# Performance work log

Hardware: AMD Instinct MI355X
Metric: run time of the kernel (lower is better)

The kernel has to match this reference:

```python
import jax, jax.numpy as jnp
import numpy as np

N, E, G = 100000, 800000, 64
F_IN, H = 92, 4
D1, D2, D3 = 32, 64, 128  # per-head out dims: hidden//2, hidden, 2*hidden
HID, LAT = 64, 128
FINAL = H * D3  # 512
NEG_SLOPE = 0.2


def _p(key, shape, scale=0.05):
    return jax.random.normal(key, shape, dtype=jnp.float32) * scale


def setup_inputs() -> dict:
    key = jax.random.key(0)
    ks = jax.random.split(key, 32)
    node_feat = jax.random.normal(ks[0], (N, F_IN), dtype=jnp.float32)
    src = jax.random.randint(ks[1], (E,), 0, N)
    dst = jax.random.randint(ks[2], (E,), 0, N)
    graph_id = jnp.sort(jax.random.randint(ks[3], (N,), 0, G))
    d = {"node_feat": node_feat, "src": src, "dst": dst, "graph_id": graph_id}
    # GAT layer params (DGL GATConv: fc no bias, attn_l/attn_r [H,D], bias [H*D])
    dims = [(F_IN, D1), (H * D1, D2), (H * D2, D3)]
    i = 4
    for li, (fi, do) in enumerate(dims, 1):
        d[f"W{li}"] = _p(ks[i], (fi, H * do)); i += 1
        d[f"al{li}"] = _p(ks[i], (H, do)); i += 1
        d[f"ar{li}"] = _p(ks[i], (H, do)); i += 1
        d[f"b{li}"] = jnp.zeros((H * do,), dtype=jnp.float32)
    # gate MLP: Linear(final, hid) -> ReLU -> Linear(hid, 1)
    d["Wg1"] = _p(ks[i], (FINAL, HID)); i += 1
    d["bg1"] = jnp.zeros((HID,), dtype=jnp.float32)
    d["Wg2"] = _p(ks[i], (HID, 1)); i += 1
    d["bg2"] = jnp.zeros((1,), dtype=jnp.float32)
    d["Wmu"] = _p(ks[i], (FINAL, LAT)); i += 1
    d["bmu"] = jnp.zeros((LAT,), dtype=jnp.float32)
    d["Wlv"] = _p(ks[i], (FINAL, LAT)); i += 1
    d["blv"] = jnp.zeros((LAT,), dtype=jnp.float32)
    return d


def gat_layer(h, W, al, ar, b, src, dst, heads, d_out):
    n = h.shape[0]
    Wh = (h @ W).reshape(n, heads, d_out)                      # [N,H,D]
    el = jnp.einsum('nhd,hd->nh', Wh, al)                      # a_l . Wh
    er = jnp.einsum('nhd,hd->nh', Wh, ar)
    e = jax.nn.leaky_relu(el[src] + er[dst], NEG_SLOPE)        # [E,H]
    m = jax.ops.segment_max(e, dst, num_segments=n)
    m = jnp.where(jnp.isfinite(m), m, 0.0)                     # zero-in-degree guard
    ex = jnp.exp(e - m[dst])
    s = jax.ops.segment_sum(ex, dst, num_segments=n)
    a = ex / jnp.maximum(s[dst], 1e-9)                         # edge softmax
    msg = a[:, :, None] * Wh[src]                              # [E,H,D] (peak intermediate)
    out = jax.ops.segment_sum(msg, dst, num_segments=n)        # scatter-aggregate
    out = out + b.reshape(1, heads, d_out)
    return out.reshape(n, heads * d_out)                       # flatten(1)


def attention_pool(h, graph_id, Wg1, bg1, Wg2, bg2, num_graphs):
    gate = jax.nn.relu(h @ Wg1 + bg1) @ Wg2 + bg2              # [N,1]
    m = jax.ops.segment_max(gate, graph_id, num_segments=num_graphs)
    ex = jnp.exp(gate - m[graph_id])
    s = jax.ops.segment_sum(ex, graph_id, num_segments=num_graphs)
    a = ex / jnp.maximum(s[graph_id], 1e-9)                    # softmax over nodes per graph
    return jax.ops.segment_sum(a * h, graph_id, num_segments=num_graphs)  # [G,final]


def reference(node_feat, src, dst, graph_id,
              W1, al1, ar1, b1, W2, al2, ar2, b2, W3, al3, ar3, b3,
              Wg1, bg1, Wg2, bg2, Wmu, bmu, Wlv, blv):
    h = jax.nn.elu(gat_layer(node_feat, W1, al1, ar1, b1, src, dst, H, D1))
    h = jax.nn.elu(gat_layer(h, W2, al2, ar2, b2, src, dst, H, D2))
    h = jax.nn.elu(gat_layer(h, W3, al3, ar3, b3, src, dst, H, D3))
    g = attention_pool(h, graph_id, Wg1, bg1, Wg2, bg2, G)
    mu = g @ Wmu + bmu
    logvar = g @ Wlv + blv
    return (mu, logvar)
```

## Files before the change

### kernel.cpp

```cpp
#include <hip/hip_runtime.h>
#include <math.h>

#define NNODES 100000
#define NEDGES 800000
#define NGRAPH 64
#define NHEAD  4
#define FINALD 512
#define HIDG   64
#define LATD   128
#define K1P    96
#define NB_SCAN 98

typedef unsigned int uint;
typedef unsigned short ushort;
typedef __attribute__((ext_vector_type(8))) short bf16x8;
typedef __attribute__((ext_vector_type(4))) float f32x4;

__device__ __forceinline__ float bflo(uint u) { return __uint_as_float(u << 16); }
__device__ __forceinline__ float bfhi(uint u) { return __uint_as_float(u & 0xffff0000u); }
__device__ __forceinline__ ushort f2bf(float f) {
    uint u = __float_as_uint(f);
    return (ushort)((u + 0x7fffu + ((u >> 16) & 1u)) >> 16);
}
__device__ __forceinline__ uint pack2(float a, float b) {
    return (uint)f2bf(a) | ((uint)f2bf(b) << 16);
}

__global__ void init_kernel(int* __restrict__ deg, const int* __restrict__ gid,
                            int* __restrict__ gstart) {
    int i = blockIdx.x * blockDim.x + threadIdx.x;
    if (i < NNODES) deg[i] = 0;
    if (i <= NGRAPH) {
        int lo = 0, hi = NNODES;
        while (lo < hi) {
            int mid = (lo + hi) >> 1;
            if (gid[mid] < i) lo = mid + 1; else hi = mid;
        }
        gstart[i] = lo;
    }
}
__global__ void count_kernel(const int* __restrict__ dst, int* __restrict__ deg) {
    int e = blockIdx.x * blockDim.x + threadIdx.x;
    if (e < NEDGES) atomicAdd(&deg[dst[e]], 1);
}
__global__ __launch_bounds__(1024) void scan_block_kernel(const int* __restrict__ deg,
                                                          int* __restrict__ off,
                                                          int* __restrict__ bsum) {
    __shared__ int buf[1024];
    int t = threadIdx.x;
    int i = blockIdx.x * 1024 + t;
    int x = (i < NNODES) ? deg[i] : 0;
    buf[t] = x;
    __syncthreads();
    for (int s = 1; s < 1024; s <<= 1) {
        int v = (t >= s) ? buf[t - s] : 0;
        __syncthreads();
        buf[t] += v;
        __syncthreads();
    }
    if (i < NNODES) off[i] = buf[t] - x;
    if (t == 1023) bsum[blockIdx.x] = buf[1023];
}
__global__ __launch_bounds__(128) void scan_bsum_kernel(int* __restrict__ bsum) {
    __shared__ int buf[128];
    int t = threadIdx.x;
    int x = (t < NB_SCAN) ? bsum[t] : 0;
    buf[t] = x;
    __syncthreads();
    for (int s = 1; s < 128; s <<= 1) {
        int v = (t >= s) ? buf[t - s] : 0;
        __syncthreads();
        buf[t] += v;
        __syncthreads();
    }
    if (t < NB_SCAN) bsum[t] = buf[t] - x;
    if (t == 0) bsum[NB_SCAN] = buf[NB_SCAN - 1];
}
__global__ __launch_bounds__(1024) void scan_add_kernel(int* __restrict__ off,
                                                        const int* __restrict__ bsum,
                                                        int* __restrict__ cursor) {
    int i = blockIdx.x * 1024 + threadIdx.x;
    if (i < NNODES) {
        int v = off[i] + bsum[blockIdx.x];
        off[i] = v;
        cursor[i] = v;
    }
    if (i == 0) off[NNODES] = bsum[NB_SCAN];
}
__global__ void scatter_kernel(const int* __restrict__ src, const int* __restrict__ dst,
                               int* __restrict__ cursor, int* __restrict__ src_csr) {
    int e = blockIdx.x * blockDim.x + threadIdx.x;
    if (e >= NEDGES) return;
    int p = atomicAdd(&cursor[dst[e]], 1);
    src_csr[p] = src[e];
}

#define C1 (128 * K1P)
#define C2 (256 * 128)
#define C3 (512 * 256)
#define CG (64 * 512)
#define CX (NNODES * K1P)
#define CTOT (C1 + C2 + C3 + CG + CX + NNODES)
__global__ void conv_all_kernel(const float* __restrict__ W1, const float* __restrict__ W2,
                                const float* __restrict__ W3, const float* __restrict__ Wg1,
                                const float* __restrict__ nf,
                                ushort* __restrict__ Bt1, ushort* __restrict__ Bt2,
                                ushort* __restrict__ Bt3, ushort* __restrict__ Btg,
                                ushort* __restrict__ x0, float* __restrict__ gate) {
    int i = blockIdx.x * blockDim.x + threadIdx.x;
    if (i < C1) {
        int n = i / K1P, k = i - n * K1P;
        Bt1[i] = (k < 92) ? f2bf(W1[(size_t)k * 128 + n]) : (ushort)0;
        return;
    }
    i -= C1;
    if (i < C2) {
        int n = i >> 7, k = i & 127;
        Bt2[i] = f2bf(W2[(size_t)k * 256 + n]);
        return;
    }
    i -= C2;
    if (i < C3) {
        int n = i >> 8, k = i & 255;
        Bt3[i] = f2bf(W3[(size_t)k * 512 + n]);
        return;
    }
    i -= C3;
    if (i < CG) {
        int n = i >> 9, k = i & 511;
        Btg[i] = f2bf(Wg1[(size_t)k * 64 + n]);
        return;
    }
    i -= CG;
    if (i < CX) {
        int n = i / K1P, k = i - n * K1P;
        x0[i] = (k < 92) ? f2bf(nf[(size_t)n * 92 + k]) : (ushort)0;
        return;
    }
    i -= CX;
    if (i < NNODES) gate[i] = 0.f;
}

template <int BN, int MODE>
__global__ __launch_bounds__(256) void mfma_gemm(const ushort* __restrict__ A,
                                                 const ushort* __restrict__ Bt,
                                                 const float* __restrict__ bias,
                                                 ushort* __restrict__ C,
                                                 const float* __restrict__ Wg2,
                                                 float* __restrict__ gate,
                                                 int M, int K, int N) {
    constexpr int WNS = BN / 2;
    constexpr int NT = WNS / 16;
    __shared__ ushort Alds[128][40];
    __shared__ ushort Blds[BN][40];
    int tid = threadIdx.x;
    int wave = tid >> 6, lane = tid & 63;
    int wm = wave & 1, wn = wave >> 1;
    int quad = lane >> 4, l16 = lane & 15;
    int rowBase = blockIdx.y * 128;
    int colBase = blockIdx.x * BN;

    f32x4 acc[4][NT];
#pragma unroll
    for (int i = 0; i < 4; i++)
#pragma unroll
        for (int j = 0; j < NT; j++) acc[i][j] = (f32x4){0.f, 0.f, 0.f, 0.f};

    for (int k0 = 0; k0 < K; k0 += 32) {
        {
            int r = tid >> 1;
            int c0 = (tid & 1) * 8;
            int row = rowBase + r;
            uint4 v0 = make_uint4(0u, 0u, 0u, 0u);
            uint4 v1 = make_uint4(0u, 0u, 0u, 0u);
            if (row < M) {
                const ushort* ap = &A[(size_t)row * K + k0];
                v0 = *(const uint4*)&ap[c0];
                v1 = *(const uint4*)&ap[c0 + 16];
            }
            *(uint4*)&Alds[r][c0] = v0;
            *(uint4*)&Alds[r][c0 + 16] = v1;
        }
        if constexpr (BN == 128) {
            int r = tid >> 1;
            int c0 = (tid & 1) * 8;
            const ushort* bp = &Bt[(size_t)(colBase + r) * K + k0];
            *(uint4*)&Blds[r][c0] = *(const uint4*)&bp[c0];
            *(uint4*)&Blds[r][c0 + 16] = *(const uint4*)&bp[c0 + 16];
        } else {
            int r = tid >> 2, ch = tid & 3;
            uint4 v = *(const uint4*)&Bt[(size_t)(colBase + r) * K + k0 + ch * 8];
            *(uint4*)&Blds[r][ch * 8] = v;
        }
        __syncthreads();
        bf16x8 af[4], bf[NT];
#pragma unroll
        for (int i = 0; i < 4; i++)
            af[i] = *(const bf16x8*)&Alds[wm * 64 + i * 16 + l16][quad * 8];
#pragma unroll
        for (int j = 0; j < NT; j++)
            bf[j] = *(const bf16x8*)&Blds[wn * WNS + j * 16 + l16][quad * 8];
#pragma unroll
        for (int i = 0; i < 4; i++)
#pragma unroll
            for (int j = 0; j < NT; j++)
                acc[i][j] = __builtin_amdgcn_mfma_f32_16x16x32_bf16(af[i], bf[j], acc[i][j], 0, 0, 0);
        __syncthreads();
    }

    if constexpr (MODE == 0) {
#pragma unroll
        for (int i = 0; i < 4; i++) {
#pragma unroll
            for (int j = 0; j < NT; j++) {
                int col = colBase + wn * WNS + j * 16 + l16;
#pragma unroll
                for (int r = 0; r < 4; r++) {
                    int row = rowBase + wm * 64 + i * 16 + quad * 4 + r;
                    if (row < M) C[(size_t)row * N + col] = f2bf(acc[i][j][r]);
                }
            }
        }
    } else {
        float bb[NT], wg[NT];
#pragma unroll
        for (int j = 0; j < NT; j++) {
            int col = colBase + wn * WNS + j * 16 + l16;
            bb[j] = bias[col];
            wg[j] = Wg2[col];
        }
#pragma unroll
        for (int i = 0; i < 4; i++) {
            float pd[4] = {0.f, 0.f, 0.f, 0.f};
#pragma unroll
            for (int j = 0; j < NT; j++) {
#pragma unroll
                for (int r = 0; r < 4; r++) {
                    float x = fmaxf(acc[i][j][r] + bb[j], 0.f);
                    pd[r] = fmaf(x, wg[j], pd[r]);
                }
            }
#pragma unroll
            for (int m = 1; m < 16; m <<= 1)
#pragma unroll
                for (int r = 0; r < 4; r++)
                    pd[r] += __shfl_xor(pd[r], m, 64);
            if (l16 == 0) {
#pragma unroll
                for (int r = 0; r < 4; r++) {
                    int row = rowBase + wm * 64 + i * 16 + quad * 4 + r;
                    if (row < M) atomicAdd(&gate[row], pd[r]);
                }
            }
        }
    }
}

template <int HD>
__global__ __launch_bounds__(256) void eler_node(const ushort* __restrict__ Wh,
                                                 const float* __restrict__ al,
                                                 const float* __restrict__ ar,
                                                 float* __restrict__ el,
                                                 float* __restrict__ er) {
    constexpr int D = HD / NHEAD;
    constexpr int LPN = HD / 8;
    constexpr int S = D / 8;
    int n = blockIdx.x * 4 + (threadIdx.x >> 6);
    int lane = threadIdx.x & 63;
    float sl = 0.f, sr = 0.f;
    if (lane < LPN) {
        int d0 = lane * 8;
        uint4 v = *(const uint4*)&Wh[(size_t)n * HD + d0];
        float w0 = bflo(v.x), w1 = bfhi(v.x), w2 = bflo(v.y), w3 = bfhi(v.y);
        float w4 = bflo(v.z), w5 = bfhi(v.z), w6 = bflo(v.w), w7 = bfhi(v.w);
        float4 a0 = *(const float4*)&al[d0];
        float4 a1 = *(const float4*)&al[d0 + 4];
        float4 b0 = *(const float4*)&ar[d0];
        float4 b1 = *(const float4*)&ar[d0 + 4];
        sl = w0 * a0.x; sl = fmaf(w1, a0.y, sl); sl = fmaf(w2, a0.z, sl); sl = fmaf(w3, a0.w, sl);
        sl = fmaf(w4, a1.x, sl); sl = fmaf(w5, a1.y, sl); sl = fmaf(w6, a1.z, sl); sl = fmaf(w7, a1.w, sl);
        sr = w0 * b0.x; sr = fmaf(w1, b0.y, sr); sr = fmaf(w2, b0.z, sr); sr = fmaf(w3, b0.w, sr);
        sr = fmaf(w4, b1.x, sr); sr = fmaf(w5, b1.y, sr); sr = fmaf(w6, b1.z, sr); sr = fmaf(w7, b1.w, sr);
    }
#pragma unroll
    for (int o = S / 2; o > 0; o >>= 1) {
        sl += __shfl_down(sl, o, 64);
        sr += __shfl_down(sr, o, 64);
    }
    if (lane < LPN && (lane % S) == 0) {
        int h = lane / S;
        el[n * 4 + h] = sl;
        er[n * 4 + h] = sr;
    }
}

__global__ void attn_node(const int* __restrict__ src_csr, const int* __restrict__ off,
                          const float4* __restrict__ el4, const float4* __restrict__ er4,
                          float4* __restrict__ aw4, float4* __restrict__ nsum4) {
    int n = blockIdx.x * blockDim.x + threadIdx.x;
    if (n >= NNODES) return;
    int i0 = off[n], i1 = off[n + 1];
    float4 ern = er4[n];
    float m0 = -1e30f, m1 = -1e30f, m2 = -1e30f, m3 = -1e30f;
    for (int i = i0; i < i1; i += 8) {
        int cnt = i1 - i; if (cnt > 8) cnt = 8;
        int s8[8];
#pragma unroll
        for (int j = 0; j < 8; j++)
            if (j < cnt) s8[j] = src_csr[i + j];
        float4 e8[8];
#pragma unroll
        for (int j = 0; j < 8; j++)
            if (j < cnt) e8[j] = el4[s8[j]];
#pragma unroll
        for (int j = 0; j < 8; j++) {
            if (j < cnt) {
                float4 x = e8[j];
                x.x += ern.x; x.y += ern.y; x.z += ern.z; x.w += ern.w;
                x.x = (x.x >= 0.f) ? x.x : 0.2f * x.x;
                x.y = (x.y >= 0.f) ? x.y : 0.2f * x.y;
                x.z = (x.z >= 0.f) ? x.z : 0.2f * x.z;
                x.w = (x.w >= 0.f) ? x.w : 0.2f * x.w;
                aw4[i + j] = x;
                m0 = fmaxf(m0, x.x); m1 = fmaxf(m1, x.y);
                m2 = fmaxf(m2, x.z); m3 = fmaxf(m3, x.w);
            }
        }
    }
    float4 s = make_float4(0.f, 0.f, 0.f, 0.f);
    for (int i = i0; i < i1; i++) {
        float4 x = aw4[i];
        x.x = expf(x.x - m0); x.y = expf(x.y - m1);
        x.z = expf(x.z - m2); x.w = expf(x.w - m3);
        s.x += x.x; s.y += x.y; s.z += x.z; s.w += x.w;
        aw4[i] = x;
    }
    nsum4[n] = s;
}

__global__ __launch_bounds__(256) void gat_aggregate(const int* __restrict__ src_csr,
                                                     const int* __restrict__ off,
                                                     const ushort* __restrict__ Wh,
                                                     const float* __restrict__ aw,
                                                     const float* __restrict__ nsum,
                                                     const float* __restrict__ bias,
                                                     ushort* __restrict__ out,
                                                     int HD, int logHD8, int logD, int total8) {
    int idx = blockIdx.x * blockDim.x + threadIdx.x;
    if (idx >= total8) return;
    int n = idx >> logHD8;
    int d = (idx & ((1 << logHD8) - 1)) << 3;
    int h = d >> logD;
    int i0 = off[n], i1 = off[n + 1];
    float acc[8] = {0.f, 0.f, 0.f, 0.f, 0.f, 0.f, 0.f, 0.f};
    for (int i = i0; i < i1; i += 8) {
        int cnt = i1 - i; if (cnt > 8) cnt = 8;
        int s8[8]; float w8[8];
#pragma unroll
        for (int j = 0; j < 8; j++) {
            if (j < cnt) {
                s8[j] = src_csr[i + j];
                w8[j] = aw[(i + j) * 4 + h];
            }
        }
#pragma unroll
        for (int j = 0; j < 8; j++) {
            if (j < cnt) {
                uint4 v = *(const uint4*)&Wh[(size_t)s8[j] * HD + d];
                float w = w8[j];
                acc[0] = fmaf(w, bflo(v.x), acc[0]);
                acc[1] = fmaf(w, bfhi(v.x), acc[1]);
                acc[2] = fmaf(w, bflo(v.y), acc[2]);
                acc[3] = fmaf(w, bfhi(v.y), acc[3]);
                acc[4] = fmaf(w, bflo(v.z), acc[4]);
                acc[5] = fmaf(w, bfhi(v.z), acc[5]);
                acc[6] = fmaf(w, bflo(v.w), acc[6]);
                acc[7] = fmaf(w, bfhi(v.w), acc[7]);
            }
        }
    }
    float inv = 1.f / fmaxf(nsum[n * 4 + h], 1e-9f);
    float r[8];
#pragma unroll
    for (int j = 0; j < 8; j++) {
        float x = acc[j] * inv + bias[d + j];
        r[j] = (x > 0.f) ? x : (expf(x) - 1.f);
    }
    uint4 o;
    o.x = pack2(r[0], r[1]);
    o.y = pack2(r[2], r[3]);
    o.z = pack2(r[4], r[5]);
    o.w = pack2(r[6], r[7]);
    *(uint4*)&out[(size_t)n * HD + d] = o;
}

__global__ __launch_bounds__(256) void graph_softmax_kernel(const float* __restrict__ gate,
                                                            const int* __restrict__ gstart,
                                                            float* __restrict__ exn,
                                                            float* __restrict__ gsum) {
    int g = blockIdx.x, t = threadIdx.x;
    int n0 = gstart[g], n1 = gstart[g + 1];
    __shared__ float red[256];
    float m = -1e30f;
    for (int n = n0 + t; n < n1; n += 256) m = fmaxf(m, gate[n]);
    red[t] = m; __syncthreads();
    for (int s = 128; s > 0; s >>= 1) {
        if (t < s) red[t] = fmaxf(red[t], red[t + s]);
        __syncthreads();
    }
    m = red[0]; __syncthreads();
    float sum = 0.f;
    for (int n = n0 + t; n < n1; n += 256) {
        float v = expf(gate[n] - m);
        exn[n] = v;
        sum += v;
    }
    red[t] = sum; __syncthreads();
    for (int s = 128; s > 0; s >>= 1) {
        if (t < s) red[t] += red[t + s];
        __syncthreads();
    }
    if (t == 0) gsum[g] = red[0];
}

__global__ __launch_bounds__(128) void pool_partial(const ushort* __restrict__ h,
                                                    const float* __restrict__ exn,
                                                    const int* __restrict__ gstart,
                                                    float* __restrict__ partial) {
    int g = blockIdx.x, q = blockIdx.y;
    int n0 = gstart[g], n1 = gstart[g + 1];
    int len = n1 - n0;
    int chunk = (len + 3) >> 2;
    int s = n0 + q * chunk;
    int e = s + chunk; if (e > n1) e = n1;
    int d4 = threadIdx.x;
    const uint2* h2 = (const uint2*)h;
    float a0 = 0.f, a1 = 0.f, a2 = 0.f, a3 = 0.f;
    for (int n = s; n < e; n++) {
        float w = exn[n];
        uint2 v = h2[(size_t)n * 128 + d4];
        a0 = fmaf(w, bflo(v.x), a0);
        a1 = fmaf(w, bfhi(v.x), a1);
        a2 = fmaf(w, bflo(v.y), a2);
        a3 = fmaf(w, bfhi(v.y), a3);
    }
    *(float4*)&partial[((size_t)(g * 4 + q)) * FINALD + d4 * 4] = make_float4(a0, a1, a2, a3);
}

__global__ __launch_bounds__(128) void final_kernel(const float* __restrict__ partial,
                                                    const float* __restrict__ gsum,
                                                    const float* __restrict__ Wmu,
                                                    const float* __restrict__ bmu,
                                                    const float* __restrict__ Wlv,
                                                    const float* __restrict__ blv,
                                                    float* __restrict__ out) {
    int g = blockIdx.x, j = threadIdx.x;
    const float* p = partial + (size_t)g * 4 * FINALD;
    float am = 0.f, av = 0.f;
    for (int k = 0; k < FINALD; k++) {
        float pv = p[k] + p[FINALD + k] + p[2 * FINALD + k] + p[3 * FINALD + k];
        am = fmaf(pv, Wmu[k * LATD + j], am);
        av = fmaf(pv, Wlv[k * LATD + j], av);
    }
    float inv = 1.f / fmaxf(gsum[g], 1e-9f);
    out[g * LATD + j] = am * inv + bmu[j];
    out[NGRAPH * LATD + g * LATD + j] = av * inv + blv[j];
}

extern "C" void kernel_launch(void* const* d_in, const int* in_sizes, int n_in,
                              void* d_out, int out_size, void* d_ws, size_t ws_size,
                              hipStream_t stream) {
    (void)in_sizes; (void)n_in; (void)out_size; (void)ws_size;
    const float* node_feat = (const float*)d_in[0];
    const int* src = (const int*)d_in[1];
    const int* dst = (const int*)d_in[2];
    const int* gid = (const int*)d_in[3];
    const float* W[3]    = {(const float*)d_in[4],  (const float*)d_in[8],  (const float*)d_in[12]};
    const float* al[3]   = {(const float*)d_in[5],  (const float*)d_in[9],  (const float*)d_in[13]};
    const float* ar[3]   = {(const float*)d_in[6],  (const float*)d_in[10], (const float*)d_in[14]};
    const float* bias[3] = {(const float*)d_in[7],  (const float*)d_in[11], (const float*)d_in[15]};
    const float* Wg1 = (const float*)d_in[16];
    const float* bg1 = (const float*)d_in[17];
    const float* Wg2 = (const float*)d_in[18];
    const float* Wmu = (const float*)d_in[20];
    const float* bmu = (const float*)d_in[21];
    const float* Wlv = (const float*)d_in[22];
    const float* blv = (const float*)d_in[23];

    char* ws = (char*)d_ws;
    size_t woff = 0;
    auto carve = [&](size_t bytes) {
        void* p = ws + woff;
        woff = (woff + bytes + 255) & ~(size_t)255;
        return p;
    };
    ushort* hA      = (ushort*)carve((size_t)NNODES * 512 * 2);
    ushort* hB      = (ushort*)carve((size_t)NNODES * 512 * 2);
    float*  el      = (float*) carve((size_t)NNODES * 4 * 4);
    float*  er      = (float*) carve((size_t)NNODES * 4 * 4);
    float*  aw      = (float*) carve((size_t)NEDGES * 4 * 4);
    float*  nsum    = (float*) carve((size_t)NNODES * 4 * 4);
    int*    deg     = (int*)   carve((size_t)NNODES * 4);
    int*    off     = (int*)   carve((size_t)(NNODES + 1) * 4);
    int*    cursor  = (int*)   carve((size_t)NNODES * 4);
    int*    src_csr = (int*)   carve((size_t)NEDGES * 4);
    int*    bsum    = (int*)   carve((size_t)(NB_SCAN + 1) * 4);
    float*  gate    = (float*) carve((size_t)NNODES * 4);
    float*  exn     = (float*) carve((size_t)NNODES * 4);
    int*    gstart  = (int*)   carve((size_t)(NGRAPH + 1) * 4);
    float*  partial = (float*) carve((size_t)NGRAPH * 4 * FINALD * 4);
    float*  gsum    = (float*) carve((size_t)NGRAPH * 4);
    ushort* Bt1     = (ushort*)carve((size_t)128 * K1P * 2);
    ushort* Bt2     = (ushort*)carve((size_t)256 * 128 * 2);
    ushort* Bt3     = (ushort*)carve((size_t)512 * 256 * 2);
    ushort* Btg     = (ushort*)carve((size_t)64 * 512 * 2);
    ushort* x0      = hA;

    init_kernel<<<(NNODES + 255) / 256, 256, 0, stream>>>(deg, gid, gstart);
    count_kernel<<<(NEDGES + 255) / 256, 256, 0, stream>>>(dst, deg);
    scan_block_kernel<<<NB_SCAN, 1024, 0, stream>>>(deg, off, bsum);
    scan_bsum_kernel<<<1, 128, 0, stream>>>(bsum);
    scan_add_kernel<<<NB_SCAN, 1024, 0, stream>>>(off, bsum, cursor);
    scatter_kernel<<<(NEDGES + 255) / 256, 256, 0, stream>>>(src, dst, cursor, src_csr);
    conv_all_kernel<<<(CTOT + 255) / 256, 256, 0, stream>>>(
        W[0], W[1], W[2], Wg1, node_feat, Bt1, Bt2, Bt3, Btg, x0, gate);

    const int HDs[3]    = {128, 256, 512};
    const int logHD8[3] = {4, 5, 6};
    const int logD[3]   = {5, 6, 7};
    const int MB = (NNODES + 127) / 128;

    for (int l = 0; l < 3; l++) {
        int HD = HDs[l];
        if (l == 0)
            mfma_gemm<128, 0><<<dim3(1, MB), 256, 0, stream>>>(
                x0, Bt1, nullptr, hB, nullptr, nullptr, NNODES, K1P, 128);
        else if (l == 1)
            mfma_gemm<128, 0><<<dim3(2, MB), 256, 0, stream>>>(
                hA, Bt2, nullptr, hB, nullptr, nullptr, NNODES, 128, 256);
        else
            mfma_gemm<128, 0><<<dim3(4, MB), 256, 0, stream>>>(
                hA, Bt3, nullptr, hB, nullptr, nullptr, NNODES, 256, 512);
        if (l == 0)      eler_node<128><<<NNODES / 4, 256, 0, stream>>>(hB, al[l], ar[l], el, er);
        else if (l == 1) eler_node<256><<<NNODES / 4, 256, 0, stream>>>(hB, al[l], ar[l], el, er);
        else             eler_node<512><<<NNODES / 4, 256, 0, stream>>>(hB, al[l], ar[l], el, er);
        attn_node<<<(NNODES + 255) / 256, 256, 0, stream>>>(
            src_csr, off, (const float4*)el, (const float4*)er, (float4*)aw, (float4*)nsum);
        int total8 = NNODES * (HD / 8);
        gat_aggregate<<<(total8 + 255) / 256, 256, 0, stream>>>(
            src_csr, off, hB, aw, nsum, bias[l], hA, HD, logHD8[l], logD[l], total8);
    }

    mfma_gemm<64, 1><<<dim3(1, MB), 256, 0, stream>>>(
        hA, Btg, bg1, nullptr, Wg2, gate, NNODES, FINALD, HIDG);
    graph_softmax_kernel<<<NGRAPH, 256, 0, stream>>>(gate, gstart, exn, gsum);
    pool_partial<<<dim3(NGRAPH, 4), 128, 0, stream>>>(hA, exn, gstart, partial);
    final_kernel<<<NGRAPH, 128, 0, stream>>>(partial, gsum, Wmu, bmu, Wlv, blv, (float*)d_out);
}
```

Measured before the change: 889.0 us.

## Fuse edge softmax into aggregation with wave-per-node online softmax; widen pool split

Replaces the separate attn_node and gat_aggregate kernels with one attn_aggregate kernel that assigns a 64-lane wavefront to each destination node. The wave computes per-head max and sum with an online softmax and shuffle reductions, then recomputes edge weights on the fly while gathering neighbor features. This removes the per-edge attention buffer and its write/read round trip. Separately, the graph pooling is split into 16 partial chunks per graph instead of 4 to raise parallelism, with final_kernel reducing them through shared memory. The cost is recomputing exp and el gathers per lane, and lower per-thread work for small head dims.

```diff
diff --git a/kernel.cpp b/kernel.cpp
--- a/kernel.cpp
+++ b/kernel.cpp
@@ -10,6 +10,7 @@
 #define LATD   128
 #define K1P    96
 #define NB_SCAN 98
+#define PQ     16
 
 typedef unsigned int uint;
 typedef unsigned short ushort;
@@ -24,6 +25,9 @@
 }
 __device__ __forceinline__ uint pack2(float a, float b) {
     return (uint)f2bf(a) | ((uint)f2bf(b) << 16);
+}
+__device__ __forceinline__ float selh(float4 v, int h) {
+    return (h & 2) ? ((h & 1) ? v.w : v.z) : ((h & 1) ? v.y : v.x);
 }
 
 __global__ void init_kernel(int* __restrict__ deg, const int* __restrict__ gid,
@@ -294,104 +298,119 @@
     }
 }
 
-__global__ void attn_node(const int* __restrict__ src_csr, const int* __restrict__ off,
-                          const float4* __restrict__ el4, const float4* __restrict__ er4,
-                          float4* __restrict__ aw4, float4* __restrict__ nsum4) {
-    int n = blockIdx.x * blockDim.x + threadIdx.x;
-    if (n >= NNODES) return;
+template <int HD>
+__global__ __launch_bounds__(256) void attn_aggregate(const int* __restrict__ src_csr,
+                                                      const int* __restrict__ off,
+                                                      const ushort* __restrict__ Wh,
+                                                      const float4* __restrict__ el4,
+                                                      const float4* __restrict__ er4,
+                                                      const float* __restrict__ bias,
+                                                      ushort* __restrict__ out) {
+    constexpr int DPL = HD / 64;
+    int n = blockIdx.x * 4 + (threadIdx.x >> 6);
+    int lane = threadIdx.x & 63;
     int i0 = off[n], i1 = off[n + 1];
     float4 ern = er4[n];
-    float m0 = -1e30f, m1 = -1e30f, m2 = -1e30f, m3 = -1e30f;
-    for (int i = i0; i < i1; i += 8) {
-        int cnt = i1 - i; if (cnt > 8) cnt = 8;
-        int s8[8];
-#pragma unroll
-        for (int j = 0; j < 8; j++)
-            if (j < cnt) s8[j] = src_csr[i + j];
-        float4 e8[8];
-#pragma unroll
-        for (int j = 0; j < 8; j++)
-            if (j < cnt) e8[j] = el4[s8[j]];
-#pragma unroll
-        for (int j = 0; j < 8; j++) {
-            if (j < cnt) {
-                float4 x = e8[j];
-                x.x += ern.x; x.y += ern.y; x.z += ern.z; x.w += ern.w;
-                x.x = (x.x >= 0.f) ? x.x : 0.2f * x.x;
-                x.y = (x.y >= 0.f) ? x.y : 0.2f * x.y;
-                x.z = (x.z >= 0.f) ? x.z : 0.2f * x.z;
-                x.w = (x.w >= 0.f) ? x.w : 0.2f * x.w;
-                aw4[i + j] = x;
-                m0 = fmaxf(m0, x.x); m1 = fmaxf(m1, x.y);
-                m2 = fmaxf(m2, x.z); m3 = fmaxf(m3, x.w);
-            }
-        }
-    }
-    float4 s = make_float4(0.f, 0.f, 0.f, 0.f);
-    for (int i = i0; i < i1; i++) {
-        float4 x = aw4[i];
-        x.x = expf(x.x - m0); x.y = expf(x.y - m1);
-        x.z = expf(x.z - m2); x.w = expf(x.w - m3);
-        s.x += x.x; s.y += x.y; s.z += x.z; s.w += x.w;
-        aw4[i] = x;
-    }
-    nsum4[n] = s;
-}
-
-__global__ __launch_bounds__(256) void gat_aggregate(const int* __restrict__ src_csr,
-                                                     const int* __restrict__ off,
-                                                     const ushort* __restrict__ Wh,
-                                                     const float* __restrict__ aw,
-                                                     const float* __restrict__ nsum,
-                                                     const float* __restrict__ bias,
-                                                     ushort* __restrict__ out,
-                                                     int HD, int logHD8, int logD, int total8) {
-    int idx = blockIdx.x * blockDim.x + threadIdx.x;
-    if (idx >= total8) return;
-    int n = idx >> logHD8;
-    int d = (idx & ((1 << logHD8) - 1)) << 3;
-    int h = d >> logD;
-    int i0 = off[n], i1 = off[n + 1];
-    float acc[8] = {0.f, 0.f, 0.f, 0.f, 0.f, 0.f, 0.f, 0.f};
+
+    float m[4] = {-1e30f, -1e30f, -1e30f, -1e30f};
+    float s[4] = {0.f, 0.f, 0.f, 0.f};
+    for (int i = i0 + lane; i < i1; i += 64) {
+        float4 x = el4[src_csr[i]];
+        float xs[4] = {x.x + ern.x, x.y + ern.y, x.z + ern.z, x.w + ern.w};
+#pragma unroll
+        for (int c = 0; c < 4; c++) {
+            float v = (xs[c] >= 0.f) ? xs[c] : 0.2f * xs[c];
+            float M = fmaxf(m[c], v);
+            s[c] = s[c] * expf(m[c] - M) + expf(v - M);
+            m[c] = M;
+        }
+    }
+    float gm[4] = {m[0], m[1], m[2], m[3]};
+#pragma unroll
+    for (int o = 1; o < 64; o <<= 1)
+#pragma unroll
+        for (int c = 0; c < 4; c++)
+            gm[c] = fmaxf(gm[c], __shfl_xor(gm[c], o, 64));
+#pragma unroll
+    for (int c = 0; c < 4; c++) s[c] *= expf(m[c] - gm[c]);
+#pragma unroll
+    for (int o = 1; o < 64; o <<= 1)
+#pragma unroll
+        for (int c = 0; c < 4; c++)
+            s[c] += __shfl_xor(s[c], o, 64);
+
+    int h = (lane * DPL) / (HD / 4);
+    float mh  = (h & 2) ? ((h & 1) ? gm[3] : gm[2]) : ((h & 1) ? gm[1] : gm[0]);
+    float sh  = (h & 2) ? ((h & 1) ? s[3] : s[2]) : ((h & 1) ? s[1] : s[0]);
+    float erh = selh(ern, h);
+    float inv = 1.f / fmaxf(sh, 1e-9f);
+
+    int d = lane * DPL;
+    float acc[DPL];
+#pragma unroll
+    for (int j = 0; j < DPL; j++) acc[j] = 0.f;
     for (int i = i0; i < i1; i += 8) {
         int cnt = i1 - i; if (cnt > 8) cnt = 8;
         int s8[8]; float w8[8];
 #pragma unroll
+        for (int j = 0; j < 8; j++)
+            if (j < cnt) s8[j] = src_csr[i + j];
+#pragma unroll
         for (int j = 0; j < 8; j++) {
             if (j < cnt) {
-                s8[j] = src_csr[i + j];
-                w8[j] = aw[(i + j) * 4 + h];
+                float xs = selh(el4[s8[j]], h) + erh;
+                xs = (xs >= 0.f) ? xs : 0.2f * xs;
+                w8[j] = expf(xs - mh) * inv;
             }
         }
 #pragma unroll
         for (int j = 0; j < 8; j++) {
             if (j < cnt) {
-                uint4 v = *(const uint4*)&Wh[(size_t)s8[j] * HD + d];
+                const ushort* p = &Wh[(size_t)s8[j] * HD + d];
                 float w = w8[j];
-                acc[0] = fmaf(w, bflo(v.x), acc[0]);
-                acc[1] = fmaf(w, bfhi(v.x), acc[1]);
-                acc[2] = fmaf(w, bflo(v.y), acc[2]);
-                acc[3] = fmaf(w, bfhi(v.y), acc[3]);
-                acc[4] = fmaf(w, bflo(v.z), acc[4]);
-                acc[5] = fmaf(w, bfhi(v.z), acc[5]);
-                acc[6] = fmaf(w, bflo(v.w), acc[6]);
-                acc[7] = fmaf(w, bfhi(v.w), acc[7]);
+                if constexpr (DPL == 8) {
+                    uint4 v = *(const uint4*)p;
+                    acc[0] = fmaf(w, bflo(v.x), acc[0]);
+                    acc[1] = fmaf(w, bfhi(v.x), acc[1]);
+                    acc[2] = fmaf(w, bflo(v.y), acc[2]);
+                    acc[3] = fmaf(w, bfhi(v.y), acc[3]);
+                    acc[4] = fmaf(w, bflo(v.z), acc[4]);
+                    acc[5] = fmaf(w, bfhi(v.z), acc[5]);
+                    acc[6] = fmaf(w, bflo(v.w), acc[6]);
+                    acc[7] = fmaf(w, bfhi(v.w), acc[7]);
+                } else if constexpr (DPL == 4) {
+                    uint2 v = *(const uint2*)p;
+                    acc[0] = fmaf(w, bflo(v.x), acc[0]);
+                    acc[1] = fmaf(w, bfhi(v.x), acc[1]);
+                    acc[2] = fmaf(w, bflo(v.y), acc[2]);
+                    acc[3] = fmaf(w, bfhi(v.y), acc[3]);
+                } else {
+                    uint v = *(const uint*)p;
+                    acc[0] = fmaf(w, bflo(v), acc[0]);
+                    acc[1] = fmaf(w, bfhi(v), acc[1]);
+                }
             }
         }
     }
-    float inv = 1.f / fmaxf(nsum[n * 4 + h], 1e-9f);
-    float r[8];
-#pragma unroll
-    for (int j = 0; j < 8; j++) {
-        float x = acc[j] * inv + bias[d + j];
+    float r[DPL];
+#pragma unroll
+    for (int j = 0; j < DPL; j++) {
+        float x = acc[j] + bias[d + j];
         r[j] = (x > 0.f) ? x : (expf(x) - 1.f);
     }
-    uint4 o;
-    o.x = pack2(r[0], r[1]);
-    o.y = pack2(r[2], r[3]);
-    o.z = pack2(r[4], r[5]);
-    o.w = pack2(r[6], r[7]);
-    *(uint4*)&out[(size_t)n * HD + d] = o;
+    ushort* po = &out[(size_t)n * HD + d];
+    if constexpr (DPL == 8) {
+        uint4 o;
+        o.x = pack2(r[0], r[1]); o.y = pack2(r[2], r[3]);
+        o.z = pack2(r[4], r[5]); o.w = pack2(r[6], r[7]);
+        *(uint4*)po = o;
+    } else if constexpr (DPL == 4) {
+        uint2 o;
+        o.x = pack2(r[0], r[1]); o.y = pack2(r[2], r[3]);
+        *(uint2*)po = o;
+    } else {
+        *(uint*)po = pack2(r[0], r[1]);
+    }
 }
 
 __global__ __launch_bounds__(256) void graph_softmax_kernel(const float* __restrict__ gate,
@@ -430,7 +449,7 @@
     int g = blockIdx.x, q = blockIdx.y;
     int n0 = gstart[g], n1 = gstart[g + 1];
     int len = n1 - n0;
-    int chunk = (len + 3) >> 2;
+    int chunk = (len + PQ - 1) / PQ;
     int s = n0 + q * chunk;
     int e = s + chunk; if (e > n1) e = n1;
     int d4 = threadIdx.x;
@@ -444,7 +463,7 @@
         a2 = fmaf(w, bflo(v.y), a2);
         a3 = fmaf(w, bfhi(v.y), a3);
     }
-    *(float4*)&partial[((size_t)(g * 4 + q)) * FINALD + d4 * 4] = make_float4(a0, a1, a2, a3);
+    *(float4*)&partial[((size_t)(g * PQ + q)) * FINALD + d4 * 4] = make_float4(a0, a1, a2, a3);
 }
 
 __global__ __launch_bounds__(128) void final_kernel(const float* __restrict__ partial,
@@ -455,10 +474,18 @@
                                                     const float* __restrict__ blv,
                                                     float* __restrict__ out) {
     int g = blockIdx.x, j = threadIdx.x;
-    const float* p = partial + (size_t)g * 4 * FINALD;
+    __shared__ float pooled[FINALD];
+    const float* p = partial + (size_t)g * PQ * FINALD;
+    for (int k = j; k < FINALD; k += 128) {
+        float v = 0.f;
+#pragma unroll
+        for (int q = 0; q < PQ; q++) v += p[q * FINALD + k];
+        pooled[k] = v;
+    }
+    __syncthreads();
     float am = 0.f, av = 0.f;
     for (int k = 0; k < FINALD; k++) {
-        float pv = p[k] + p[FINALD + k] + p[2 * FINALD + k] + p[3 * FINALD + k];
+        float pv = pooled[k];
         am = fmaf(pv, Wmu[k * LATD + j], am);
         av = fmaf(pv, Wlv[k * LATD + j], av);
     }
@@ -498,8 +525,6 @@
     ushort* hB      = (ushort*)carve((size_t)NNODES * 512 * 2);
     float*  el      = (float*) carve((size_t)NNODES * 4 * 4);
     float*  er      = (float*) carve((size_t)NNODES * 4 * 4);
-    float*  aw      = (float*) carve((size_t)NEDGES * 4 * 4);
-    float*  nsum    = (float*) carve((size_t)NNODES * 4 * 4);
     int*    deg     = (int*)   carve((size_t)NNODES * 4);
     int*    off     = (int*)   carve((size_t)(NNODES + 1) * 4);
     int*    cursor  = (int*)   carve((size_t)NNODES * 4);
@@ -508,7 +533,7 @@
     float*  gate    = (float*) carve((size_t)NNODES * 4);
     float*  exn     = (float*) carve((size_t)NNODES * 4);
     int*    gstart  = (int*)   carve((size_t)(NGRAPH + 1) * 4);
-    float*  partial = (float*) carve((size_t)NGRAPH * 4 * FINALD * 4);
+    float*  partial = (float*) carve((size_t)NGRAPH * PQ * FINALD * 4);
     float*  gsum    = (float*) carve((size_t)NGRAPH * 4);
     ushort* Bt1     = (ushort*)carve((size_t)128 * K1P * 2);
     ushort* Bt2     = (ushort*)carve((size_t)256 * 128 * 2);
@@ -525,35 +550,34 @@
     conv_all_kernel<<<(CTOT + 255) / 256, 256, 0, stream>>>(
         W[0], W[1], W[2], Wg1, node_feat, Bt1, Bt2, Bt3, Btg, x0, gate);
 
-    const int HDs[3]    = {128, 256, 512};
-    const int logHD8[3] = {4, 5, 6};
-    const int logD[3]   = {5, 6, 7};
     const int MB = (NNODES + 127) / 128;
+    const int NWB = NNODES / 4;
 
     for (int l = 0; l < 3; l++) {
-        int HD = HDs[l];
-        if (l == 0)
+        if (l == 0) {
             mfma_gemm<128, 0><<<dim3(1, MB), 256, 0, stream>>>(
                 x0, Bt1, nullptr, hB, nullptr, nullptr, NNODES, K1P, 128);
-        else if (l == 1)
+            eler_node<128><<<NWB, 256, 0, stream>>>(hB, al[0], ar[0], el, er);
+            attn_aggregate<128><<<NWB, 256, 0, stream>>>(
+                src_csr, off, hB, (const float4*)el, (const float4*)er, bias[0], hA);
+        } else if (l == 1) {
             mfma_gemm<128, 0><<<dim3(2, MB), 256, 0, stream>>>(
                 hA, Bt2, nullptr, hB, nullptr, nullptr, NNODES, 128, 256);
-        else
+            eler_node<256><<<NWB, 256, 0, stream>>>(hB, al[1], ar[1], el, er);
+            attn_aggregate<256><<<NWB, 256, 0, stream>>>(
+                src_csr, off, hB, (const float4*)el, (const float4*)er, bias[1], hA);
+        } else {
             mfma_gemm<128, 0><<<dim3(4, MB), 256, 0, stream>>>(
                 hA, Bt3, nullptr, hB, nullptr, nullptr, NNODES, 256, 512);
-        if (l == 0)      eler_node<128><<<NNODES / 4, 256, 0, stream>>>(hB, al[l], ar[l], el, er);
-        else if (l == 1) eler_node<256><<<NNODES / 4, 256, 0, stream>>>(hB, al[l], ar[l], el, er);
-        else             eler_node<512><<<NNODES / 4, 256, 0, stream>>>(hB, al[l], ar[l], el, er);
-        attn_node<<<(NNODES + 255) / 256, 256, 0, stream>>>(
-            src_csr, off, (const float4*)el, (const float4*)er, (float4*)aw, (float4*)nsum);
-        int total8 = NNODES * (HD / 8);
-        gat_aggregate<<<(total8 + 255) / 256, 256, 0, stream>>>(
-            src_csr, off, hB, aw, nsum, bias[l], hA, HD, logHD8[l], logD[l], total8);
+            eler_node<512><<<NWB, 256, 0, stream>>>(hB, al[2], ar[2], el, er);
+            attn_aggregate<512><<<NWB, 256, 0, stream>>>(
+                src_csr, off, hB, (const float4*)el, (const float4*)er, bias[2], hA);
+        }
     }
 
     mfma_gemm<64, 1><<<dim3(1, MB), 256, 0, stream>>>(
         hA, Btg, bg1, nullptr, Wg2, gate, NNODES, FINALD, HIDG);
     graph_softmax_kernel<<<NGRAPH, 256, 0, stream>>>(gate, gstart, exn, gsum);
-    pool_partial<<<dim3(NGRAPH, 4), 128, 0, stream>>>(hA, exn, gstart, partial);
+    pool_partial<<<dim3(NGRAPH, PQ), 128, 0, stream>>>(hA, exn, gstart, partial);
     final_kernel<<<NGRAPH, 128, 0, stream>>>(partial, gsum, Wmu, bmu, Wlv, blv, (float*)d_out);
 }
```

Measured after the change: 1.018 ms. 1.15x slower.
